# Optimization experiments

Hardware: AMD Instinct MI355X
Metric: run time of the kernel (lower is better)

## Reference

```python
import jax, jax.numpy as jnp
import numpy as np
from jax import lax

IMAGE_SIZE = 1280
STRIDE = 32
FMP = IMAGE_SIZE // STRIDE          # 40
BPC = 5                             # boxes per cell (5 anchors)
NUM_CLASSES = 80
NMS_THRESH = 0.5
CONF_THRESH = 0.3
N_BOX = FMP * FMP * BPC             # 8000 candidates
ANCHOR_SIZE = np.array([[17, 25], [55, 75], [92, 206], [202, 21], [289, 311]], dtype=np.float32)


def _make_anchors():
    # generate_anchors: per-cell (x,y) grid repeated for each of BPC anchors, tiled anchor wh
    ys, xs = jnp.meshgrid(jnp.arange(FMP, dtype=jnp.float32), jnp.arange(FMP, dtype=jnp.float32), indexing='ij')
    xy = jnp.stack([xs, ys], axis=-1).reshape(-1, 1, 2)                       # [HW,1,2]
    anchor_xy = jnp.broadcast_to(xy, (FMP * FMP, BPC, 2)).reshape(-1, 2)      # [N,2]
    anchor_wh = jnp.broadcast_to(jnp.asarray(ANCHOR_SIZE)[None], (FMP * FMP, BPC, 2)).reshape(-1, 2)
    return jnp.concatenate([anchor_xy, anchor_wh], axis=-1)                   # [N,4]


def setup_inputs() -> dict:
    key = jax.random.key(0)
    k = jax.random.split(key, 5)
    return {
        'cls_feat': jax.random.normal(k[0], (1, 512, FMP, FMP), jnp.float32),
        'reg_feat': jax.random.normal(k[1], (1, 512, FMP, FMP), jnp.float32),
        'w_obj': jax.random.normal(k[2], (BPC, 512), jnp.float32) * 0.02,
        'b_obj': jnp.zeros((BPC,), jnp.float32),
        'w_cls': jax.random.normal(k[3], (NUM_CLASSES * BPC, 512), jnp.float32) * 0.02,
        'b_cls': jnp.zeros((NUM_CLASSES * BPC,), jnp.float32),
        'w_reg': jax.random.normal(k[4], (4 * BPC, 512), jnp.float32) * 0.02,
        'b_reg': jnp.zeros((4 * BPC,), jnp.float32),
    }


def reference(cls_feat, reg_feat, w_obj, b_obj, w_cls, b_cls, w_reg, b_reg):
    # 1x1 convs as channel contractions, already permuted to NHWC like permute(0,2,3,1)
    obj = (jnp.einsum('bchw,oc->bhwo', reg_feat, w_obj) + b_obj).reshape(-1, 1)            # [N,1]
    cls = (jnp.einsum('bchw,oc->bhwo', cls_feat, w_cls) + b_cls).reshape(-1, NUM_CLASSES)  # [N,C]
    reg = (jnp.einsum('bchw,oc->bhwo', reg_feat, w_reg) + b_reg).reshape(-1, 4)            # [N,4]

    scores = jnp.sqrt(jax.nn.sigmoid(obj) * jax.nn.sigmoid(cls))                           # [N,C]

    # decode_boxes
    anchors = _make_anchors()
    ctr = (jax.nn.sigmoid(reg[:, :2]) + anchors[:, :2]) * STRIDE
    wh = jnp.exp(reg[:, 2:]) * anchors[:, 2:]
    bboxes = jnp.concatenate([ctr - wh * 0.5, ctr + wh * 0.5], axis=-1)                    # [N,4] x1y1x2y2

    # postprocess: per-box best class + confidence filter
    labels = jnp.argmax(scores, axis=1)
    score = jnp.take_along_axis(scores, labels[:, None], axis=1)[:, 0]
    valid = score >= CONF_THRESH

    # faithful to original nms(): it re-interprets decoded x1y1x2y2 as cxcywh before IoU
    b2 = jnp.concatenate([bboxes[:, :2] - bboxes[:, 2:] * 0.5,
                          bboxes[:, :2] + bboxes[:, 2:] * 0.5], axis=-1)

    # greedy per-class NMS == global greedy with cross-class IoU gated to 0
    order = jnp.argsort(-score)
    bs = b2[order]
    ls = labels[order]
    vs = valid[order]
    areas = (bs[:, 2] - bs[:, 0]) * (bs[:, 3] - bs[:, 1])
    xx1 = jnp.maximum(bs[:, None, 0], bs[None, :, 0])
    yy1 = jnp.maximum(bs[:, None, 1], bs[None, :, 1])
    xx2 = jnp.minimum(bs[:, None, 2], bs[None, :, 2])
    yy2 = jnp.minimum(bs[:, None, 3], bs[None, :, 3])
    inter = jnp.maximum(1e-10, xx2 - xx1) * jnp.maximum(1e-10, yy2 - yy1)
    iou = inter / (areas[:, None] + areas[None, :] - inter + 1e-14)                        # [N,N]
    same = ls[:, None] == ls[None, :]

    idx = jnp.arange(N_BOX)

    def body(k, supp):
        active = vs[k] & jnp.logical_not(supp[k])
        row = active & (iou[k] > NMS_THRESH) & same[k] & (idx > k)
        return supp | row

    supp = lax.fori_loop(0, N_BOX, body, jnp.zeros(N_BOX, bool))
    keep = jnp.zeros(N_BOX, bool).at[order].set(vs & jnp.logical_not(supp))

    # fixed-size masked outputs (original returns variable-length filtered arrays)
    return bboxes, score, labels, keep
```

## Files before the change

### kernel.cpp

```cpp
#include <hip/hip_runtime.h>
#include <math.h>

#define FMPX 40
#define NPOS 1600
#define NCLS 80
#define NBOX 8000
#define KDIM 512
#define KC   64
#define CAP  256

__constant__ float c_aw[5] = {17.f, 55.f, 92.f, 202.f, 289.f};
__constant__ float c_ah[5] = {25.f, 75.f, 206.f, 21.f, 311.f};

__device__ __forceinline__ float sigf(float x) { return 1.0f / (1.0f + expf(-x)); }

__global__ __launch_bounds__(256) void k_gemm(
    const float* __restrict__ cls_feat, const float* __restrict__ reg_feat,
    const float* __restrict__ w_obj, const float* __restrict__ b_obj,
    const float* __restrict__ w_cls, const float* __restrict__ b_cls,
    const float* __restrict__ w_reg, const float* __restrict__ b_reg,
    float* __restrict__ clsRaw,
    float* __restrict__ roRaw)
{
    __shared__ float Ws[16 * KDIM];
    __shared__ float As[KC * 64];
    const int mTile = blockIdx.x;
    const int nTile = blockIdx.y;
    const int hw0   = mTile * 64;
    const bool isCls = (nTile < 25);
    const float* feat = isCls ? cls_feat : reg_feat;

    const int pos = threadIdx.x & 63;
    const int og  = threadIdx.x >> 6;

    for (int i = threadIdx.x * 4; i < 16 * KDIM; i += 256 * 4) {
        int r = i >> 9, k = i & 511;
        const float* src;
        bool valid = true;
        if (isCls) {
            src = w_cls + (nTile * 16 + r) * KDIM + k;
        } else {
            int o = (nTile - 25) * 16 + r;
            if (o < 5)       src = w_obj + o * KDIM + k;
            else if (o < 25) src = w_reg + (o - 5) * KDIM + k;
            else           { src = w_obj; valid = false; }
        }
        float4 v = valid ? *(const float4*)src : make_float4(0.f, 0.f, 0.f, 0.f);
        *(float4*)&Ws[i] = v;
    }

    float bias[4];
    bool ok[4];
#pragma unroll
    for (int j = 0; j < 4; j++) {
        int r = og * 4 + j;
        if (isCls) {
            bias[j] = b_cls[nTile * 16 + r]; ok[j] = true;
        } else {
            int o = (nTile - 25) * 16 + r;
            if (o < 5)       { bias[j] = b_obj[o];     ok[j] = true; }
            else if (o < 25) { bias[j] = b_reg[o - 5]; ok[j] = true; }
            else             { bias[j] = 0.0f;         ok[j] = false; }
        }
    }

    float acc[4] = {0.f, 0.f, 0.f, 0.f};
    const float* wsBase = &Ws[(og * 4) * KDIM];

    for (int kc = 0; kc < KDIM; kc += KC) {
        for (int i = threadIdx.x * 4; i < KC * 64; i += 256 * 4) {
            int r = i >> 6, c = i & 63;
            *(float4*)&As[i] = *(const float4*)&feat[(kc + r) * NPOS + hw0 + c];
        }
        __syncthreads();

        for (int kk = 0; kk < KC; kk += 8) {
            float a[8];
#pragma unroll
            for (int t = 0; t < 8; t++) a[t] = As[(kk + t) * 64 + pos];
#pragma unroll
            for (int j = 0; j < 4; j++) {
                const float* wp = wsBase + j * KDIM + kc + kk;
                float4 wA = *(const float4*)wp;
                float4 wB = *(const float4*)(wp + 4);
                acc[j] += a[0] * wA.x; acc[j] += a[1] * wA.y;
                acc[j] += a[2] * wA.z; acc[j] += a[3] * wA.w;
                acc[j] += a[4] * wB.x; acc[j] += a[5] * wB.y;
                acc[j] += a[6] * wB.z; acc[j] += a[7] * wB.w;
            }
        }
        __syncthreads();
    }

    const int hw = hw0 + pos;
    if (isCls) {
        float4 rv = make_float4(acc[0] + bias[0], acc[1] + bias[1],
                                acc[2] + bias[2], acc[3] + bias[3]);
        *(float4*)&clsRaw[hw * 400 + nTile * 16 + og * 4] = rv;
    } else {
#pragma unroll
        for (int j = 0; j < 4; j++) {
            int o = (nTile - 25) * 16 + og * 4 + j;
            if (ok[j]) roRaw[hw * 25 + o] = acc[j] + bias[j];
        }
    }
}

__global__ __launch_bounds__(256) void k_box(
    const float* __restrict__ clsRaw, const float* __restrict__ roRaw,
    float* __restrict__ out,
    float4* __restrict__ nmsBox, float* __restrict__ nmsArea,
    float* __restrict__ listScore, int* __restrict__ listIdx, int* __restrict__ counts)
{
    const int n = blockIdx.x * 4 + (threadIdx.x >> 6);
    const int lane = threadIdx.x & 63;
    const int hw = n / 5, a = n % 5;

    const float sobj = sigf(roRaw[hw * 25 + a]);
    const float* cbase = clsRaw + hw * 400 + a * 80;

    float v = sqrtf(sobj * sigf(cbase[lane]));
    int bi = lane;
    if (lane < 16) {
        float s2 = sqrtf(sobj * sigf(cbase[64 + lane]));
        if (s2 > v) { v = s2; bi = 64 + lane; }
    }
#pragma unroll
    for (int off = 32; off >= 1; off >>= 1) {
        float ov = __shfl_xor(v, off);
        int   oi = __shfl_xor(bi, off);
        if (ov > v || (ov == v && oi < bi)) { v = ov; bi = oi; }
    }

    if (lane == 0) {
        const float* rp = roRaw + hw * 25 + 5 + a * 4;
        float r0 = rp[0], r1 = rp[1], r2 = rp[2], r3 = rp[3];
        float gx = (float)(hw % FMPX), gy = (float)(hw / FMPX);
        float cx = (sigf(r0) + gx) * 32.0f;
        float cy = (sigf(r1) + gy) * 32.0f;
        float wv = expf(r2) * c_aw[a];
        float hv = expf(r3) * c_ah[a];
        float x1 = cx - wv * 0.5f, y1 = cy - hv * 0.5f;
        float x2 = cx + wv * 0.5f, y2 = cy + hv * 0.5f;

        out[n * 4 + 0] = x1; out[n * 4 + 1] = y1;
        out[n * 4 + 2] = x2; out[n * 4 + 3] = y2;
        out[32000 + n] = v;
        out[40000 + n] = (float)bi;
        out[48000 + n] = 0.0f;

        float nx1 = x1 - x2 * 0.5f, ny1 = y1 - y2 * 0.5f;
        float nx2 = x1 + x2 * 0.5f, ny2 = y1 + y2 * 0.5f;
        nmsBox[n]  = make_float4(nx1, ny1, nx2, ny2);
        nmsArea[n] = (nx2 - nx1) * (ny2 - ny1);

        if (v >= 0.3f) {
            int p = atomicAdd(&counts[bi], 1);
            if (p < CAP) { listScore[bi * CAP + p] = v; listIdx[bi * CAP + p] = n; }
        }
    }
}

__global__ __launch_bounds__(64) void k_nms(
    const float* __restrict__ listScore, const int* __restrict__ listIdx,
    const int* __restrict__ counts,
    const float4* __restrict__ nmsBox, const float* __restrict__ nmsArea,
    float* __restrict__ keepOut)
{
    const int c = blockIdx.x;
    int m = counts[c];
    if (m > CAP) m = CAP;

    int P = 2;
    while (P < m) P <<= 1;

    __shared__ float ss[CAP];
    __shared__ int   si[CAP];
    __shared__ float bx1[CAP], by1[CAP], bx2[CAP], by2[CAP], bar[CAP];
    __shared__ int   supp[CAP];

    for (int i = threadIdx.x; i < P; i += 64) {
        if (i < m) { ss[i] = listScore[c * CAP + i]; si[i] = listIdx[c * CAP + i]; }
        else       { ss[i] = -INFINITY;              si[i] = 0x7FFFFFFF; }
    }
    __syncthreads();

    for (int size = 2; size <= P; size <<= 1) {
        for (int stride = size >> 1; stride > 0; stride >>= 1) {
            for (int t = threadIdx.x; t < P / 2; t += 64) {
                int lo = 2 * stride * (t / stride) + (t % stride);
                int hi = lo + stride;
                bool desc = ((lo & size) == 0);
                float slo = ss[lo], shi = ss[hi];
                int   ilo = si[lo], ihi = si[hi];
                bool loBetter = (slo > shi) || (slo == shi && ilo < ihi);
                bool doSwap = desc ? !loBetter : loBetter;
                if (doSwap) { ss[lo] = shi; ss[hi] = slo; si[lo] = ihi; si[hi] = ilo; }
            }
            __syncthreads();
        }
    }

    for (int i = threadIdx.x; i < m; i += 64) {
        int n = si[i];
        float4 b = nmsBox[n];
        bx1[i] = b.x; by1[i] = b.y; bx2[i] = b.z; by2[i] = b.w;
        bar[i] = nmsArea[n];
        supp[i] = 0;
    }
    __syncthreads();

    for (int k = 0; k < m; k++) {
        if (!supp[k]) {
            float kx1 = bx1[k], ky1 = by1[k], kx2 = bx2[k], ky2 = by2[k], ka = bar[k];
            for (int j = k + 1 + threadIdx.x; j < m; j += 64) {
                float xx1 = fmaxf(kx1, bx1[j]);
                float yy1 = fmaxf(ky1, by1[j]);
                float xx2 = fminf(kx2, bx2[j]);
                float yy2 = fminf(ky2, by2[j]);
                float inter = fmaxf(1e-10f, xx2 - xx1) * fmaxf(1e-10f, yy2 - yy1);
                float iou = inter / ((ka + bar[j] - inter) + 1e-14f);
                if (iou > 0.5f) supp[j] = 1;
            }
        }
        __syncthreads();
    }

    for (int j = threadIdx.x; j < m; j += 64) {
        if (!supp[j]) keepOut[si[j]] = 1.0f;
    }
}

extern "C" void kernel_launch(void* const* d_in, const int* in_sizes, int n_in,
                              void* d_out, int out_size, void* d_ws, size_t ws_size,
                              hipStream_t stream) {
    const float* cls_feat = (const float*)d_in[0];
    const float* reg_feat = (const float*)d_in[1];
    const float* w_obj    = (const float*)d_in[2];
    const float* b_obj    = (const float*)d_in[3];
    const float* w_cls    = (const float*)d_in[4];
    const float* b_cls    = (const float*)d_in[5];
    const float* w_reg    = (const float*)d_in[6];
    const float* b_reg    = (const float*)d_in[7];

    float* out = (float*)d_out;
    float* ws  = (float*)d_ws;

    float*  clsRaw    = ws;
    float*  roRaw     = ws + 640000;
    float4* nmsBox    = (float4*)(ws + 680000);
    float*  nmsArea   = ws + 712000;
    float*  listScore = ws + 720000;
    int*    listIdx   = (int*)(ws + 740480);
    int*    counts    = (int*)(ws + 760960);

    hipMemsetAsync(counts, 0, NCLS * sizeof(int), stream);

    k_gemm<<<dim3(25, 27), 256, 0, stream>>>(cls_feat, reg_feat,
                                             w_obj, b_obj, w_cls, b_cls, w_reg, b_reg,
                                             clsRaw, roRaw);
    k_box<<<NBOX / 4, 256, 0, stream>>>(clsRaw, roRaw, out, nmsBox, nmsArea,
                                        listScore, listIdx, counts);
    k_nms<<<NCLS, 64, 0, stream>>>(listScore, listIdx, counts, nmsBox, nmsArea,
                                   out + 48000);
}
```

Measured before the change: 184.8 us.

## Read GEMM weights via scalar loads and build per-class NMS lists inside NMS kernel

```diff
diff --git a/kernel.cpp b/kernel.cpp
--- a/kernel.cpp
+++ b/kernel.cpp
@@ -22,7 +22,6 @@
     float* __restrict__ clsRaw,
     float* __restrict__ roRaw)
 {
-    __shared__ float Ws[16 * KDIM];
     __shared__ float As[KC * 64];
     const int mTile = blockIdx.x;
     const int nTile = blockIdx.y;
@@ -31,41 +30,25 @@
     const float* feat = isCls ? cls_feat : reg_feat;
 
     const int pos = threadIdx.x & 63;
-    const int og  = threadIdx.x >> 6;
-
-    for (int i = threadIdx.x * 4; i < 16 * KDIM; i += 256 * 4) {
-        int r = i >> 9, k = i & 511;
-        const float* src;
-        bool valid = true;
-        if (isCls) {
-            src = w_cls + (nTile * 16 + r) * KDIM + k;
-        } else {
-            int o = (nTile - 25) * 16 + r;
-            if (o < 5)       src = w_obj + o * KDIM + k;
-            else if (o < 25) src = w_reg + (o - 5) * KDIM + k;
-            else           { src = w_obj; valid = false; }
-        }
-        float4 v = valid ? *(const float4*)src : make_float4(0.f, 0.f, 0.f, 0.f);
-        *(float4*)&Ws[i] = v;
-    }
-
+    const int og = __builtin_amdgcn_readfirstlane(threadIdx.x >> 6);
+
+    const float* wrow[4];
     float bias[4];
     bool ok[4];
 #pragma unroll
     for (int j = 0; j < 4; j++) {
-        int r = og * 4 + j;
         if (isCls) {
-            bias[j] = b_cls[nTile * 16 + r]; ok[j] = true;
+            int o = nTile * 16 + og * 4 + j;
+            wrow[j] = w_cls + o * KDIM; bias[j] = b_cls[o]; ok[j] = true;
         } else {
-            int o = (nTile - 25) * 16 + r;
-            if (o < 5)       { bias[j] = b_obj[o];     ok[j] = true; }
-            else if (o < 25) { bias[j] = b_reg[o - 5]; ok[j] = true; }
-            else             { bias[j] = 0.0f;         ok[j] = false; }
+            int o = (nTile - 25) * 16 + og * 4 + j;
+            if (o < 5)       { wrow[j] = w_obj + o * KDIM;       bias[j] = b_obj[o];     ok[j] = true; }
+            else if (o < 25) { wrow[j] = w_reg + (o - 5) * KDIM; bias[j] = b_reg[o - 5]; ok[j] = true; }
+            else             { wrow[j] = w_obj;                  bias[j] = 0.0f;         ok[j] = false; }
         }
     }
 
     float acc[4] = {0.f, 0.f, 0.f, 0.f};
-    const float* wsBase = &Ws[(og * 4) * KDIM];
 
     for (int kc = 0; kc < KDIM; kc += KC) {
         for (int i = threadIdx.x * 4; i < KC * 64; i += 256 * 4) {
@@ -74,19 +57,18 @@
         }
         __syncthreads();
 
+#pragma unroll
         for (int kk = 0; kk < KC; kk += 8) {
             float a[8];
 #pragma unroll
             for (int t = 0; t < 8; t++) a[t] = As[(kk + t) * 64 + pos];
 #pragma unroll
             for (int j = 0; j < 4; j++) {
-                const float* wp = wsBase + j * KDIM + kc + kk;
-                float4 wA = *(const float4*)wp;
-                float4 wB = *(const float4*)(wp + 4);
-                acc[j] += a[0] * wA.x; acc[j] += a[1] * wA.y;
-                acc[j] += a[2] * wA.z; acc[j] += a[3] * wA.w;
-                acc[j] += a[4] * wB.x; acc[j] += a[5] * wB.y;
-                acc[j] += a[6] * wB.z; acc[j] += a[7] * wB.w;
+                const float* wp = wrow[j] + kc + kk;
+                acc[j] += a[0] * wp[0]; acc[j] += a[1] * wp[1];
+                acc[j] += a[2] * wp[2]; acc[j] += a[3] * wp[3];
+                acc[j] += a[4] * wp[4]; acc[j] += a[5] * wp[5];
+                acc[j] += a[6] * wp[6]; acc[j] += a[7] * wp[7];
             }
         }
         __syncthreads();
@@ -109,8 +91,7 @@
 __global__ __launch_bounds__(256) void k_box(
     const float* __restrict__ clsRaw, const float* __restrict__ roRaw,
     float* __restrict__ out,
-    float4* __restrict__ nmsBox, float* __restrict__ nmsArea,
-    float* __restrict__ listScore, int* __restrict__ listIdx, int* __restrict__ counts)
+    float4* __restrict__ nmsBox, float* __restrict__ nmsArea)
 {
     const int n = blockIdx.x * 4 + (threadIdx.x >> 6);
     const int lane = threadIdx.x & 63;
@@ -153,41 +134,47 @@
         float nx2 = x1 + x2 * 0.5f, ny2 = y1 + y2 * 0.5f;
         nmsBox[n]  = make_float4(nx1, ny1, nx2, ny2);
         nmsArea[n] = (nx2 - nx1) * (ny2 - ny1);
-
-        if (v >= 0.3f) {
-            int p = atomicAdd(&counts[bi], 1);
-            if (p < CAP) { listScore[bi * CAP + p] = v; listIdx[bi * CAP + p] = n; }
-        }
-    }
-}
-
-__global__ __launch_bounds__(64) void k_nms(
-    const float* __restrict__ listScore, const int* __restrict__ listIdx,
-    const int* __restrict__ counts,
+    }
+}
+
+__global__ __launch_bounds__(256) void k_nms(
+    const float* __restrict__ score, const float* __restrict__ label,
     const float4* __restrict__ nmsBox, const float* __restrict__ nmsArea,
     float* __restrict__ keepOut)
 {
     const int c = blockIdx.x;
-    int m = counts[c];
-    if (m > CAP) m = CAP;
-
-    int P = 2;
-    while (P < m) P <<= 1;
 
     __shared__ float ss[CAP];
     __shared__ int   si[CAP];
     __shared__ float bx1[CAP], by1[CAP], bx2[CAP], by2[CAP], bar[CAP];
     __shared__ int   supp[CAP];
-
-    for (int i = threadIdx.x; i < P; i += 64) {
-        if (i < m) { ss[i] = listScore[c * CAP + i]; si[i] = listIdx[c * CAP + i]; }
-        else       { ss[i] = -INFINITY;              si[i] = 0x7FFFFFFF; }
+    __shared__ int   cnt;
+
+    if (threadIdx.x == 0) cnt = 0;
+    __syncthreads();
+
+    for (int i = threadIdx.x; i < NBOX; i += 256) {
+        float s = score[i];
+        if (s >= 0.3f && (int)label[i] == c) {
+            int p = atomicAdd(&cnt, 1);
+            if (p < CAP) { ss[p] = s; si[p] = i; }
+        }
+    }
+    __syncthreads();
+
+    int m = cnt;
+    if (m > CAP) m = CAP;
+
+    int P = 2;
+    while (P < m) P <<= 1;
+    for (int i = threadIdx.x; i < P; i += 256) {
+        if (i >= m) { ss[i] = -INFINITY; si[i] = 0x7FFFFFFF; }
     }
     __syncthreads();
 
     for (int size = 2; size <= P; size <<= 1) {
         for (int stride = size >> 1; stride > 0; stride >>= 1) {
-            for (int t = threadIdx.x; t < P / 2; t += 64) {
+            for (int t = threadIdx.x; t < P / 2; t += 256) {
                 int lo = 2 * stride * (t / stride) + (t % stride);
                 int hi = lo + stride;
                 bool desc = ((lo & size) == 0);
@@ -201,7 +188,7 @@
         }
     }
 
-    for (int i = threadIdx.x; i < m; i += 64) {
+    for (int i = threadIdx.x; i < m; i += 256) {
         int n = si[i];
         float4 b = nmsBox[n];
         bx1[i] = b.x; by1[i] = b.y; bx2[i] = b.z; by2[i] = b.w;
@@ -213,7 +200,7 @@
     for (int k = 0; k < m; k++) {
         if (!supp[k]) {
             float kx1 = bx1[k], ky1 = by1[k], kx2 = bx2[k], ky2 = by2[k], ka = bar[k];
-            for (int j = k + 1 + threadIdx.x; j < m; j += 64) {
+            for (int j = k + 1 + threadIdx.x; j < m; j += 256) {
                 float xx1 = fmaxf(kx1, bx1[j]);
                 float yy1 = fmaxf(ky1, by1[j]);
                 float xx2 = fminf(kx2, bx2[j]);
@@ -226,7 +213,7 @@
         __syncthreads();
     }
 
-    for (int j = threadIdx.x; j < m; j += 64) {
+    for (int j = threadIdx.x; j < m; j += 256) {
         if (!supp[j]) keepOut[si[j]] = 1.0f;
     }
 }
@@ -250,17 +237,11 @@
     float*  roRaw     = ws + 640000;
     float4* nmsBox    = (float4*)(ws + 680000);
     float*  nmsArea   = ws + 712000;
-    float*  listScore = ws + 720000;
-    int*    listIdx   = (int*)(ws + 740480);
-    int*    counts    = (int*)(ws + 760960);
-
-    hipMemsetAsync(counts, 0, NCLS * sizeof(int), stream);
 
     k_gemm<<<dim3(25, 27), 256, 0, stream>>>(cls_feat, reg_feat,
                                              w_obj, b_obj, w_cls, b_cls, w_reg, b_reg,
                                              clsRaw, roRaw);
-    k_box<<<NBOX / 4, 256, 0, stream>>>(clsRaw, roRaw, out, nmsBox, nmsArea,
-                                        listScore, listIdx, counts);
-    k_nms<<<NCLS, 64, 0, stream>>>(listScore, listIdx, counts, nmsBox, nmsArea,
-                                   out + 48000);
-}
+    k_box<<<NBOX / 4, 256, 0, stream>>>(clsRaw, roRaw, out, nmsBox, nmsArea);
+    k_nms<<<NCLS, 256, 0, stream>>>(out + 32000, out + 40000, nmsBox, nmsArea,
+                                    out + 48000);
+}
```

New measurement: 190.9 us. 1.03x slower.
